# Kernel tuning notes

Hardware: AMD Instinct MI355X
Metric: run time of the kernel (lower is better)

Reference implementation:

```python
import jax, jax.numpy as jnp
import numpy as np
import math

B, T, C, H = 2, 2048, 1024, 16
D = C // H  # head dim = 64

def setup_inputs() -> dict:
    key = jax.random.key(0)
    ks = jax.random.split(key, 9)
    s = 0.02
    return {
        "x": jax.random.normal(ks[0], (B, T, C), dtype=jnp.float32),
        "Wq": jax.random.normal(ks[1], (C, C), dtype=jnp.float32) * s,
        "bq": jax.random.normal(ks[2], (C,), dtype=jnp.float32) * s,
        "Wk": jax.random.normal(ks[3], (C, C), dtype=jnp.float32) * s,
        "bk": jax.random.normal(ks[4], (C,), dtype=jnp.float32) * s,
        "Wv": jax.random.normal(ks[5], (C, C), dtype=jnp.float32) * s,
        "bv": jax.random.normal(ks[6], (C,), dtype=jnp.float32) * s,
        "Wo": jax.random.normal(ks[7], (C, C), dtype=jnp.float32) * s,
        "bo": jax.random.normal(ks[8], (C,), dtype=jnp.float32) * s,
    }

def reference(x, Wq, bq, Wk, bk, Wv, bv, Wo, bo):
    # x: [B, T, C]; torch Linear is y = x @ W.T + b
    Bv_, Tv_, Cv_ = x.shape
    q = (x @ Wq.T + bq).reshape(Bv_, Tv_, H, D)
    k = (x @ Wk.T + bk).reshape(Bv_, Tv_, H, D)
    v = (x @ Wv.T + bv).reshape(Bv_, Tv_, H, D)
    scale = 1.0 / math.sqrt(D)
    # [B, H, Tq, Tk] attention scores
    att = jnp.einsum("bqhd,bkhd->bhqk", q, k) * scale
    causal = jnp.tril(jnp.ones((Tv_, Tv_), dtype=bool))  # [T, T]
    att = jnp.where(causal[None, None, :, :], att, -jnp.inf)
    att = jax.nn.softmax(att, axis=-1)
    y = jnp.einsum("bhqk,bkhd->bqhd", att, v).reshape(Bv_, Tv_, Cv_)
    return y @ Wo.T + bo
```

## Files before the change

kernel.cpp:

```cpp
#include <hip/hip_runtime.h>
#include <hip/hip_bf16.h>
#include <cstdint>
#include <cstddef>

typedef __attribute__((ext_vector_type(8))) short short8;
typedef __attribute__((ext_vector_type(4))) float f32x4;
typedef unsigned int u32;
typedef __attribute__((ext_vector_type(4))) u32 u32x4;

#define MFMA(a,b,c) __builtin_amdgcn_mfma_f32_16x16x32_bf16(a,b,c,0,0,0)

__device__ __forceinline__ void gload_lds16(const void* gptr, void* lptr) {
  __builtin_amdgcn_global_load_lds((const __attribute__((address_space(1))) u32*)gptr,
                                   (__attribute__((address_space(3))) u32*)lptr, 16, 0, 0);
}

template<int N> __device__ __forceinline__ void vm_wait() {
  asm volatile("s_waitcnt vmcnt(%0)" :: "n"(N) : "memory");
}

__device__ __forceinline__ void barrier_sync() {
  asm volatile("" ::: "memory");
  __builtin_amdgcn_s_barrier();
  asm volatile("" ::: "memory");
  __builtin_amdgcn_sched_barrier(0);
}

__device__ __forceinline__ unsigned short f2bf(float f) {
  __hip_bfloat16 h = __float2bfloat16(f);
  return *reinterpret_cast<unsigned short*>(&h);
}

__device__ __forceinline__ short8 ldg8(const unsigned short* p) {
  return *reinterpret_cast<const short8*>(p);
}

__device__ __forceinline__ u32 cvt_pk_bf16(float lo, float hi) {
  u32 r;
  asm("v_cvt_pk_bf16_f32 %0, %1, %2" : "=v"(r) : "v"(lo), "v"(hi));
  return r;
}

__global__ __launch_bounds__(256) void cvt_all_kernel(
    const float* __restrict__ x,
    const float* __restrict__ w0, const float* __restrict__ w1,
    const float* __restrict__ w2, const float* __restrict__ w3,
    unsigned short* __restrict__ xb,
    unsigned short* __restrict__ o0, unsigned short* __restrict__ o1,
    unsigned short* __restrict__ o2, unsigned short* __restrict__ o3)
{
  int id = blockIdx.x * blockDim.x + threadIdx.x;
  const float* in;
  unsigned short* out;
  int idx;
  if (id < 1048576) {
    in = x; out = xb; idx = id;
  } else {
    int r = id - 1048576;
    int z = r >> 18;
    idx = r & 262143;
    in  = (z == 0) ? w0 : (z == 1) ? w1 : (z == 2) ? w2 : w3;
    out = (z == 0) ? o0 : (z == 1) ? o1 : (z == 2) ? o2 : o3;
  }
  float4 f = reinterpret_cast<const float4*>(in)[idx];
  ushort4 o;
  o.x = f2bf(f.x); o.y = f2bf(f.y); o.z = f2bf(f.z); o.w = f2bf(f.w);
  reinterpret_cast<ushort4*>(out)[idx] = o;
}

template<int BM, int BN, int WM, int WN, bool F32OUT>
__device__ __forceinline__ void gemm2_body(
    const unsigned short* __restrict__ A,
    const unsigned short* __restrict__ W,
    const float* __restrict__ bias,
    unsigned short* __restrict__ outb, float* __restrict__ outf,
    int ldo, float oscale, int m0)
{
  constexpr int K = 1024, BK = 32, NT = K / BK;
  constexpr int NTHR = WM * WN * 64;
  constexpr int FM = BM / (WM * 16);
  constexpr int FN = BN / (WN * 16);
  constexpr int NLA = BM * BK * 2 / (NTHR * 16);
  constexpr int NLB = BN * BK * 2 / (NTHR * 16);
  constexpr int NLD = NLA + NLB;

  __shared__ unsigned short As[2][BM * BK];
  __shared__ unsigned short Ws[2][BN * BK];

  const int tid = threadIdx.x;
  const int lane = tid & 63;
  const int wave = tid >> 6;
  const int wm = wave / WN, wn = wave % WN;
  const int wr = wm * FM * 16, wc = wn * FN * 16;
  const int lr = lane >> 4, lc = lane & 15;

  f32x4 acc[FM][FN] = {};

  const char* Ab = (const char*)(A + (size_t)m0 * K);
  const char* Wb = (const char*)W;

#define STAGE(buf, k0)                                                            \
  {                                                                               \
    _Pragma("unroll")                                                             \
    for (int i = 0; i < NLA; ++i) {                                               \
      int L = (i * NTHR + tid) * 16;                                              \
      int row = L >> 6;                                                           \
      int col = L & 63;                                                           \
      gload_lds16(Ab + (size_t)row * 2048 + (k0) * 2 + col, (char*)&As[buf][0] + L); \
    }                                                                             \
    _Pragma("unroll")                                                             \
    for (int i = 0; i < NLB; ++i) {                                               \
      int L = (i * NTHR + tid) * 16;                                              \
      int row = L >> 6;                                                           \
      int col = L & 63;                                                           \
      gload_lds16(Wb + (size_t)row * 2048 + (k0) * 2 + col, (char*)&Ws[buf][0] + L); \
    }                                                                             \
  }

#define COMPUTE(buf)                                                              \
  {                                                                               \
    short8 af[FM], bf[FN];                                                        \
    _Pragma("unroll")                                                             \
    for (int m = 0; m < FM; ++m) {                                                \
      int row = wr + m * 16 + lc;                                                 \
      af[m] = *reinterpret_cast<const short8*>(                                   \
          (const char*)&As[buf][0] + row * 64 + lr * 16);                         \
    }                                                                             \
    _Pragma("unroll")                                                             \
    for (int n = 0; n < FN; ++n) {                                                \
      int row = wc + n * 16 + lc;                                                 \
      bf[n] = *reinterpret_cast<const short8*>(                                   \
          (const char*)&Ws[buf][0] + row * 64 + lr * 16);                         \
    }                                                                             \
    __builtin_amdgcn_s_setprio(1);                                                \
    _Pragma("unroll")                                                             \
    for (int m = 0; m < FM; ++m)                                                  \
      _Pragma("unroll")                                                           \
      for (int n = 0; n < FN; ++n)                                                \
        acc[m][n] = MFMA(af[m], bf[n], acc[m][n]);                                \
    __builtin_amdgcn_s_setprio(0);                                                \
  }

  STAGE(0, 0)
  STAGE(1, BK)
  int cur = 0;
#pragma unroll 1
  for (int kt = 0; kt < NT - 2; ++kt) {
    vm_wait<NLD>();
    barrier_sync();
    COMPUTE(cur)
    barrier_sync();
    STAGE(cur, (kt + 2) * BK)
    cur ^= 1;
  }
  vm_wait<NLD>();
  barrier_sync();
  COMPUTE(cur)
  cur ^= 1;
  vm_wait<0>();
  barrier_sync();
  COMPUTE(cur)

#undef STAGE
#undef COMPUTE

#pragma unroll
  for (int m = 0; m < FM; ++m)
#pragma unroll
    for (int n = 0; n < FN; ++n)
#pragma unroll
      for (int r = 0; r < 4; ++r) {
        int row = m0 + wr + m * 16 + lr * 4 + r;
        int col = wc + n * 16 + lc;
        float v = (acc[m][n][r] + bias[col]) * oscale;
        if (F32OUT) outf[(size_t)row * ldo + col] = v;
        else        outb[(size_t)row * ldo + col] = f2bf(v);
      }
}

__global__ __launch_bounds__(256, 3) void gemm_qkv5(
    const unsigned short* __restrict__ xb,
    const unsigned short* __restrict__ Wqb, const unsigned short* __restrict__ Wkb,
    const unsigned short* __restrict__ Wvb,
    const float* __restrict__ bq, const float* __restrict__ bk, const float* __restrict__ bv,
    unsigned short* __restrict__ Q, unsigned short* __restrict__ Ko, unsigned short* __restrict__ V)
{
  const int i = blockIdx.x;
  const int sw = (i & 7) * 96 + (i >> 3);
  const int z  = sw >> 8;
  const int rr = sw & 255;
  const int m0 = (rr >> 3) * 128;
  const int nr = (rr & 7) * 128;
  const unsigned short* W = ((z == 0) ? Wqb : (z == 1) ? Wkb : Wvb) + (size_t)nr * 1024;
  const float* bias = ((z == 0) ? bq : (z == 1) ? bk : bv) + nr;
  unsigned short* out = ((z == 0) ? Q : (z == 1) ? Ko : V) + nr;
  const float oscale = (z == 0) ? 0.18033688011112042f : 1.0f;
  gemm2_body<128, 128, 2, 2, false>(xb, W, bias, out, nullptr, 1024, oscale, m0);
}

__global__ __launch_bounds__(256, 2) void gemm_out3(
    const unsigned short* __restrict__ Y, const unsigned short* __restrict__ Wob,
    const float* __restrict__ bo, float* __restrict__ out)
{
  const int i = blockIdx.x;
  const int sw = (i & 7) * 64 + (i >> 3);
  const int by = sw >> 3;
  const int bx = sw & 7;
  const int m0 = by * 64;
  const int n0 = bx * 128;
  gemm2_body<64, 128, 2, 2, true>(Y, Wob + (size_t)n0 * 1024, bo + n0, nullptr, out + n0,
                                  1024, 1.0f, m0);
}

__global__ __launch_bounds__(256) void transpose_v(const unsigned short* __restrict__ V,
                                                   unsigned short* __restrict__ VT)
{
  __shared__ unsigned short tile[64 * 68];
  const int tb = blockIdx.x;
  const int bh = blockIdx.y;
  const int b = bh >> 4, h = bh & 15;
  const int tid = threadIdx.x;
  const int t0 = tb * 64;
#pragma unroll
  for (int i = 0; i < 4; ++i) {
    int e = (i * 256 + tid) * 4;
    int t = e >> 6, d = e & 63;
    ushort4 v = *reinterpret_cast<const ushort4*>(&V[((size_t)(b * 2048 + t0 + t)) * 1024 + h * 64 + d]);
    tile[t * 68 + d + 0] = v.x;
    tile[t * 68 + d + 1] = v.y;
    tile[t * 68 + d + 2] = v.z;
    tile[t * 68 + d + 3] = v.w;
  }
  __syncthreads();
#pragma unroll
  for (int i = 0; i < 4; ++i) {
    int e = (i * 256 + tid) * 4;
    int d = e >> 6, tc = e & 63;
    ushort4 w;
    w.x = tile[(tc + 0) * 68 + d];
    w.y = tile[(tc + 1) * 68 + d];
    w.z = tile[(tc + 2) * 68 + d];
    w.w = tile[(tc + 3) * 68 + d];
    *reinterpret_cast<ushort4*>(&VT[((size_t)(bh * 64 + d)) * 2048 + t0 + tc]) = w;
  }
}

__global__ __launch_bounds__(256) void attn_kernel(
    const unsigned short* __restrict__ Q, const unsigned short* __restrict__ K,
    const unsigned short* __restrict__ VT, unsigned short* __restrict__ Y)
{
  __shared__ unsigned short Ks[2][64 * 64];
  __shared__ unsigned short Vs[2][64 * 64];
  __shared__ u32 Pl[4][584];

  const int i   = blockIdx.x;
  const int xcd = i & 7;
  const int j   = i >> 3;
  const int bh  = xcd + 8 * (j & 3);
  const int qb  = 31 - (j >> 2);
  const int b = bh >> 4, h = bh & 15;
  const int tid = threadIdx.x;
  const int wave = tid >> 6;
  const int lane = tid & 63;
  const int lr = lane >> 4;
  const int lc = lane & 15;
  const float M = 4.0f;

  const unsigned short* Kbh = K + (size_t)b * 2048 * 1024 + h * 64;
  const unsigned short* Vbh = VT + (size_t)bh * 64 * 2048;
  u32* pw = Pl[wave];

  u32 ov = 0x3F803F80u;
  u32x4 ones4 = {ov, ov, ov, ov};
  short8 ones = *reinterpret_cast<short8*>(&ones4);

  const int q0 = qb * 64 + wave * 16;
  const unsigned short* qp = &Q[((size_t)(b * 2048 + q0 + lc)) * 1024 + h * 64 + lr * 8];
  short8 qa0 = ldg8(qp);
  short8 qa1 = ldg8(qp + 32);

  f32x4 o[4] = {};
  f32x4 lacc = {};

  const int nt = qb + 1;
  int cur = 0;

#pragma unroll
  for (int ii = 0; ii < 2; ++ii) {
    int L = (ii * 256 + tid) * 16;
    int row = L >> 7;
    int src = (L & 127) ^ ((row & 7) << 4);
    gload_lds16((const char*)(Kbh + (size_t)row * 1024) + src, (char*)&Ks[0][0] + L);
    gload_lds16((const char*)(Vbh + (size_t)row * 2048) + src, (char*)&Vs[0][0] + L);
  }
  __syncthreads();

  for (int t = 0; t < nt; ++t) {
    if (t + 1 < nt) {
      const int tk1 = (t + 1) * 64;
#pragma unroll
      for (int ii = 0; ii < 2; ++ii) {
        int L = (ii * 256 + tid) * 16;
        int row = L >> 7;
        int src = (L & 127) ^ ((row & 7) << 4);
        gload_lds16((const char*)(Kbh + (size_t)(tk1 + row) * 1024) + src, (char*)&Ks[cur ^ 1][0] + L);
        gload_lds16((const char*)(Vbh + (size_t)row * 2048 + tk1) + src, (char*)&Vs[cur ^ 1][0] + L);
      }
    }

    const int tk0 = t * 64;
    const unsigned short* Kt = Ks[cur];
    const unsigned short* Vt = Vs[cur];

    f32x4 s[4] = {};
#pragma unroll
    for (int kt = 0; kt < 4; ++kt) {
      int row = kt * 16 + lc;
      int sw = (row & 7) << 4;
      short8 kb0 = *reinterpret_cast<const short8*>((const char*)Kt + row * 128 + ((lr * 16) ^ sw));
      short8 kb1 = *reinterpret_cast<const short8*>((const char*)Kt + row * 128 + ((64 + lr * 16) ^ sw));
      __builtin_amdgcn_s_setprio(1);
      s[kt] = MFMA(kb0, qa0, s[kt]);
      s[kt] = MFMA(kb1, qa1, s[kt]);
      __builtin_amdgcn_s_setprio(0);
    }

    const bool diag = (t == qb);
    float p[4][4];
#pragma unroll
    for (int kt = 0; kt < 4; ++kt)
#pragma unroll
      for (int r = 0; r < 4; ++r)
        p[kt][r] = __builtin_amdgcn_exp2f(s[kt][r] - M);
    if (diag) {
#pragma unroll
      for (int kt = 0; kt < 4; ++kt)
#pragma unroll
        for (int r = 0; r < 4; ++r)
          if (tk0 + kt * 16 + lr * 4 + r > q0 + lc) p[kt][r] = 0.f;
    }

#pragma unroll
    for (int kt = 0; kt < 4; ++kt) {
      uint2 w;
      w.x = cvt_pk_bf16(p[kt][0], p[kt][1]);
      w.y = cvt_pk_bf16(p[kt][2], p[kt][3]);
      *reinterpret_cast<uint2*>(&pw[lc * 36 + kt * 8 + lr * 2]) = w;
    }
    short8 pa0 = *reinterpret_cast<const short8*>(&pw[lc * 36 + lr * 4]);
    short8 pa1 = *reinterpret_cast<const short8*>(&pw[lc * 36 + 16 + lr * 4]);

    __builtin_amdgcn_s_setprio(1);
    lacc = MFMA(pa0, ones, lacc);
    lacc = MFMA(pa1, ones, lacc);
    __builtin_amdgcn_s_setprio(0);

#pragma unroll
    for (int ntt = 0; ntt < 4; ++ntt) {
      int row = ntt * 16 + lc;
      int sw = (row & 7) << 4;
      short8 v0 = *reinterpret_cast<const short8*>((const char*)Vt + row * 128 + ((lr * 16) ^ sw));
      short8 v1 = *reinterpret_cast<const short8*>((const char*)Vt + row * 128 + ((64 + lr * 16) ^ sw));
      __builtin_amdgcn_s_setprio(1);
      o[ntt] = MFMA(pa0, v0, o[ntt]);
      o[ntt] = MFMA(pa1, v1, o[ntt]);
      __builtin_amdgcn_s_setprio(0);
    }

    __syncthreads();
    cur ^= 1;
  }

  float rl[4];
#pragma unroll
  for (int r = 0; r < 4; ++r) rl[r] = __builtin_amdgcn_rcpf(lacc[r]);
#pragma unroll
  for (int ntt = 0; ntt < 4; ++ntt)
#pragma unroll
    for (int r = 0; r < 4; ++r) {
      float val = o[ntt][r] * rl[r];
      int row = b * 2048 + q0 + lr * 4 + r;
      Y[(size_t)row * 1024 + h * 64 + ntt * 16 + lc] = f2bf(val);
    }
}

extern "C" void kernel_launch(void* const* d_in, const int* in_sizes, int n_in,
                              void* d_out, int out_size, void* d_ws, size_t ws_size,
                              hipStream_t stream)
{
  const float* x  = (const float*)d_in[0];
  const float* Wq = (const float*)d_in[1];
  const float* bq = (const float*)d_in[2];
  const float* Wk = (const float*)d_in[3];
  const float* bk = (const float*)d_in[4];
  const float* Wv = (const float*)d_in[5];
  const float* bv = (const float*)d_in[6];
  const float* Wo = (const float*)d_in[7];
  const float* bo = (const float*)d_in[8];
  float* out = (float*)d_out;

  char* ws = (char*)d_ws;
  unsigned short* xb  = (unsigned short*)(ws);
  unsigned short* Wqb = (unsigned short*)(ws + 8388608);
  unsigned short* Wkb = (unsigned short*)(ws + 8388608 + 2097152);
  unsigned short* Wvb = (unsigned short*)(ws + 8388608 + 2 * 2097152);
  unsigned short* Wob = (unsigned short*)(ws + 8388608 + 3 * 2097152);
  unsigned short* Qb  = (unsigned short*)(ws + 16777216);
  unsigned short* Kb  = (unsigned short*)(ws + 16777216 + 8388608);
  unsigned short* Vb  = (unsigned short*)(ws + 16777216 + 2 * 8388608);
  unsigned short* VTb = (unsigned short*)(ws + 16777216 + 3 * 8388608);
  unsigned short* Yb  = (unsigned short*)(ws + 16777216 + 4 * 8388608);

  cvt_all_kernel<<<8192, 256, 0, stream>>>(x, Wq, Wk, Wv, Wo, xb, Wqb, Wkb, Wvb, Wob);

  gemm_qkv5<<<768, 256, 0, stream>>>(xb, Wqb, Wkb, Wvb, bq, bk, bv, Qb, Kb, Vb);
  transpose_v<<<dim3(32, 32), 256, 0, stream>>>(Vb, VTb);
  attn_kernel<<<1024, 256, 0, stream>>>(Qb, Kb, VTb, Yb);
  gemm_out3<<<512, 256, 0, stream>>>(Yb, Wob, bo, out);
}
```

Before: 105.9 us.

## Rewrite attention with 32x32 MFMA, 128-query blocks and register P transpose

The attention kernel moves from 16x16x32 to 32x32x16 bf16 MFMA, with each wave owning 32 queries and each block 128 queries, so the grid drops from 1024 to 512 blocks. P is transposed into the B-operand layout in registers with permlane32_swap instead of going through LDS. The row sum is accumulated in scalar adds rather than a ones-MFMA. The q-block order is interleaved to balance the causal work, and launch bounds request three blocks per CU. The aim is to halve K/V LDS traffic per query and remove the LDS round trip for P. The cost is more registers per thread and fewer blocks to fill the GPU.

Measured after the change: 111.7 us. 5.5% more time.

```diff
diff --git a/kernel.cpp b/kernel.cpp
--- a/kernel.cpp
+++ b/kernel.cpp
@@ -5,10 +5,13 @@
 
 typedef __attribute__((ext_vector_type(8))) short short8;
 typedef __attribute__((ext_vector_type(4))) float f32x4;
+typedef __attribute__((ext_vector_type(16))) float f32x16;
 typedef unsigned int u32;
+typedef __attribute__((ext_vector_type(2))) u32 u32x2;
 typedef __attribute__((ext_vector_type(4))) u32 u32x4;
 
 #define MFMA(a,b,c) __builtin_amdgcn_mfma_f32_16x16x32_bf16(a,b,c,0,0,0)
+#define MFMA32(a,b,c) __builtin_amdgcn_mfma_f32_32x32x16_bf16(a,b,c,0,0,0)
 
 __device__ __forceinline__ void gload_lds16(const void* gptr, void* lptr) {
   __builtin_amdgcn_global_load_lds((const __attribute__((address_space(1))) u32*)gptr,
@@ -39,6 +42,11 @@
   u32 r;
   asm("v_cvt_pk_bf16_f32 %0, %1, %2" : "=v"(r) : "v"(lo), "v"(hi));
   return r;
+}
+
+__device__ __forceinline__ void plane32_swap(u32& a, u32& b) {
+  u32x2 r = __builtin_amdgcn_permlane32_swap(a, b, false, false);
+  a = r.x; b = r.y;
 }
 
 __global__ __launch_bounds__(256) void cvt_all_kernel(
@@ -245,143 +253,159 @@
   }
 }
 
-__global__ __launch_bounds__(256) void attn_kernel(
+__global__ __launch_bounds__(256, 3) void attn_kernel(
     const unsigned short* __restrict__ Q, const unsigned short* __restrict__ K,
     const unsigned short* __restrict__ VT, unsigned short* __restrict__ Y)
 {
   __shared__ unsigned short Ks[2][64 * 64];
   __shared__ unsigned short Vs[2][64 * 64];
-  __shared__ u32 Pl[4][584];
 
   const int i   = blockIdx.x;
   const int xcd = i & 7;
-  const int j   = i >> 3;
-  const int bh  = xcd + 8 * (j & 3);
-  const int qb  = 31 - (j >> 2);
+  const int bh  = xcd + 8 * ((i >> 3) & 3);
+  const int jj  = i >> 5;
+  const int qb  = (jj < 8) ? (15 - jj) : (jj - 8);
   const int b = bh >> 4, h = bh & 15;
   const int tid = threadIdx.x;
   const int wave = tid >> 6;
   const int lane = tid & 63;
-  const int lr = lane >> 4;
-  const int lc = lane & 15;
+  const int ql = lane & 31;
+  const int hi = lane >> 5;
   const float M = 4.0f;
 
   const unsigned short* Kbh = K + (size_t)b * 2048 * 1024 + h * 64;
   const unsigned short* Vbh = VT + (size_t)bh * 64 * 2048;
-  u32* pw = Pl[wave];
-
-  u32 ov = 0x3F803F80u;
-  u32x4 ones4 = {ov, ov, ov, ov};
-  short8 ones = *reinterpret_cast<short8*>(&ones4);
-
-  const int q0 = qb * 64 + wave * 16;
-  const unsigned short* qp = &Q[((size_t)(b * 2048 + q0 + lc)) * 1024 + h * 64 + lr * 8];
-  short8 qa0 = ldg8(qp);
-  short8 qa1 = ldg8(qp + 32);
-
-  f32x4 o[4] = {};
-  f32x4 lacc = {};
-
-  const int nt = qb + 1;
+
+  const int q0w = qb * 128 + wave * 32;
+  const int qg  = q0w + ql;
+
+  short8 qf[4];
+  {
+    const unsigned short* qp = &Q[((size_t)(b * 2048 + qg)) * 1024 + h * 64 + hi * 8];
+#pragma unroll
+    for (int kk = 0; kk < 4; ++kk) qf[kk] = ldg8(qp + kk * 16);
+  }
+
+  f32x16 o0 = {}, o1 = {};
+  float lacc = 0.f;
+
+  const int nt = 2 * qb + 2;
+
+#define STAGE_KV(buf, t)                                                          \
+  {                                                                               \
+    const int tk = (t) * 64;                                                      \
+    _Pragma("unroll")                                                             \
+    for (int ii = 0; ii < 2; ++ii) {                                              \
+      int L = (ii * 256 + tid) * 16;                                              \
+      int row = L >> 7;                                                           \
+      int src = (L & 127) ^ ((row & 7) << 4);                                     \
+      gload_lds16((const char*)(Kbh + (size_t)(tk + row) * 1024) + src,           \
+                  (char*)&Ks[buf][0] + L);                                        \
+      gload_lds16((const char*)(Vbh + (size_t)row * 2048 + tk) + src,             \
+                  (char*)&Vs[buf][0] + L);                                        \
+    }                                                                             \
+  }
+
+  STAGE_KV(0, 0)
+  __syncthreads();
   int cur = 0;
-
-#pragma unroll
-  for (int ii = 0; ii < 2; ++ii) {
-    int L = (ii * 256 + tid) * 16;
-    int row = L >> 7;
-    int src = (L & 127) ^ ((row & 7) << 4);
-    gload_lds16((const char*)(Kbh + (size_t)row * 1024) + src, (char*)&Ks[0][0] + L);
-    gload_lds16((const char*)(Vbh + (size_t)row * 2048) + src, (char*)&Vs[0][0] + L);
-  }
-  __syncthreads();
-
+#pragma unroll 1
   for (int t = 0; t < nt; ++t) {
-    if (t + 1 < nt) {
-      const int tk1 = (t + 1) * 64;
-#pragma unroll
-      for (int ii = 0; ii < 2; ++ii) {
-        int L = (ii * 256 + tid) * 16;
-        int row = L >> 7;
-        int src = (L & 127) ^ ((row & 7) << 4);
-        gload_lds16((const char*)(Kbh + (size_t)(tk1 + row) * 1024) + src, (char*)&Ks[cur ^ 1][0] + L);
-        gload_lds16((const char*)(Vbh + (size_t)row * 2048 + tk1) + src, (char*)&Vs[cur ^ 1][0] + L);
+    if (t + 1 < nt) STAGE_KV(cur ^ 1, t + 1)
+
+    const int tk0 = t * 64;
+    if (tk0 <= q0w + 31) {
+      const char* Kt = (const char*)&Ks[cur][0];
+      const char* Vt = (const char*)&Vs[cur][0];
+
+      f32x16 sa0 = {}, sa1 = {};
+#pragma unroll
+      for (int kk = 0; kk < 4; ++kk) {
+        int krow0 = ql;
+        int krow1 = 32 + ql;
+        int off = kk * 32 + hi * 16;
+        short8 ka0 = *reinterpret_cast<const short8*>(Kt + krow0 * 128 + (off ^ ((krow0 & 7) << 4)));
+        short8 ka1 = *reinterpret_cast<const short8*>(Kt + krow1 * 128 + (off ^ ((krow1 & 7) << 4)));
+        __builtin_amdgcn_s_setprio(1);
+        sa0 = MFMA32(ka0, qf[kk], sa0);
+        sa1 = MFMA32(ka1, qf[kk], sa1);
+        __builtin_amdgcn_s_setprio(0);
+      }
+
+      const bool needMask = (tk0 + 63 > q0w);
+      short8 pb[4];
+#pragma unroll
+      for (int kpos = 0; kpos < 2; ++kpos) {
+        const f32x16& sa = kpos ? sa1 : sa0;
+        const int kbase = tk0 + kpos * 32;
+        float p[16];
+#pragma unroll
+        for (int r = 0; r < 16; ++r)
+          p[r] = __builtin_amdgcn_exp2f(sa[r] - M);
+        if (needMask) {
+#pragma unroll
+          for (int r = 0; r < 16; ++r) {
+            int kg = kbase + (r & 3) + 8 * (r >> 2) + 4 * hi;
+            if (kg > qg) p[r] = 0.f;
+          }
+        }
+#pragma unroll
+        for (int r = 0; r < 16; ++r) lacc += p[r];
+        {
+          u32 a0 = cvt_pk_bf16(p[0], p[1]), b0 = cvt_pk_bf16(p[4], p[5]);
+          u32 a1 = cvt_pk_bf16(p[2], p[3]), b1 = cvt_pk_bf16(p[6], p[7]);
+          plane32_swap(a0, b0);
+          plane32_swap(a1, b1);
+          u32x4 w = {a0, a1, b0, b1};
+          pb[2 * kpos + 0] = *reinterpret_cast<short8*>(&w);
+        }
+        {
+          u32 a0 = cvt_pk_bf16(p[8], p[9]),  b0 = cvt_pk_bf16(p[12], p[13]);
+          u32 a1 = cvt_pk_bf16(p[10], p[11]), b1 = cvt_pk_bf16(p[14], p[15]);
+          plane32_swap(a0, b0);
+          plane32_swap(a1, b1);
+          u32x4 w = {a0, a1, b0, b1};
+          pb[2 * kpos + 1] = *reinterpret_cast<short8*>(&w);
+        }
+      }
+
+#pragma unroll
+      for (int kk = 0; kk < 4; ++kk) {
+        int drow0 = ql;
+        int drow1 = 32 + ql;
+        int off = kk * 32 + hi * 16;
+        short8 va0 = *reinterpret_cast<const short8*>(Vt + drow0 * 128 + (off ^ ((drow0 & 7) << 4)));
+        short8 va1 = *reinterpret_cast<const short8*>(Vt + drow1 * 128 + (off ^ ((drow1 & 7) << 4)));
+        __builtin_amdgcn_s_setprio(1);
+        o0 = MFMA32(va0, pb[kk], o0);
+        o1 = MFMA32(va1, pb[kk], o1);
+        __builtin_amdgcn_s_setprio(0);
       }
     }
 
-    const int tk0 = t * 64;
-    const unsigned short* Kt = Ks[cur];
-    const unsigned short* Vt = Vs[cur];
-
-    f32x4 s[4] = {};
-#pragma unroll
-    for (int kt = 0; kt < 4; ++kt) {
-      int row = kt * 16 + lc;
-      int sw = (row & 7) << 4;
-      short8 kb0 = *reinterpret_cast<const short8*>((const char*)Kt + row * 128 + ((lr * 16) ^ sw));
-      short8 kb1 = *reinterpret_cast<const short8*>((const char*)Kt + row * 128 + ((64 + lr * 16) ^ sw));
-      __builtin_amdgcn_s_setprio(1);
-      s[kt] = MFMA(kb0, qa0, s[kt]);
-      s[kt] = MFMA(kb1, qa1, s[kt]);
-      __builtin_amdgcn_s_setprio(0);
-    }
-
-    const bool diag = (t == qb);
-    float p[4][4];
-#pragma unroll
-    for (int kt = 0; kt < 4; ++kt)
-#pragma unroll
-      for (int r = 0; r < 4; ++r)
-        p[kt][r] = __builtin_amdgcn_exp2f(s[kt][r] - M);
-    if (diag) {
-#pragma unroll
-      for (int kt = 0; kt < 4; ++kt)
-#pragma unroll
-        for (int r = 0; r < 4; ++r)
-          if (tk0 + kt * 16 + lr * 4 + r > q0 + lc) p[kt][r] = 0.f;
-    }
-
-#pragma unroll
-    for (int kt = 0; kt < 4; ++kt) {
-      uint2 w;
-      w.x = cvt_pk_bf16(p[kt][0], p[kt][1]);
-      w.y = cvt_pk_bf16(p[kt][2], p[kt][3]);
-      *reinterpret_cast<uint2*>(&pw[lc * 36 + kt * 8 + lr * 2]) = w;
-    }
-    short8 pa0 = *reinterpret_cast<const short8*>(&pw[lc * 36 + lr * 4]);
-    short8 pa1 = *reinterpret_cast<const short8*>(&pw[lc * 36 + 16 + lr * 4]);
-
-    __builtin_amdgcn_s_setprio(1);
-    lacc = MFMA(pa0, ones, lacc);
-    lacc = MFMA(pa1, ones, lacc);
-    __builtin_amdgcn_s_setprio(0);
-
-#pragma unroll
-    for (int ntt = 0; ntt < 4; ++ntt) {
-      int row = ntt * 16 + lc;
-      int sw = (row & 7) << 4;
-      short8 v0 = *reinterpret_cast<const short8*>((const char*)Vt + row * 128 + ((lr * 16) ^ sw));
-      short8 v1 = *reinterpret_cast<const short8*>((const char*)Vt + row * 128 + ((64 + lr * 16) ^ sw));
-      __builtin_amdgcn_s_setprio(1);
-      o[ntt] = MFMA(pa0, v0, o[ntt]);
-      o[ntt] = MFMA(pa1, v1, o[ntt]);
-      __builtin_amdgcn_s_setprio(0);
-    }
-
     __syncthreads();
     cur ^= 1;
   }
 
-  float rl[4];
-#pragma unroll
-  for (int r = 0; r < 4; ++r) rl[r] = __builtin_amdgcn_rcpf(lacc[r]);
-#pragma unroll
-  for (int ntt = 0; ntt < 4; ++ntt)
-#pragma unroll
-    for (int r = 0; r < 4; ++r) {
-      float val = o[ntt][r] * rl[r];
-      int row = b * 2048 + q0 + lr * 4 + r;
-      Y[(size_t)row * 1024 + h * 64 + ntt * 16 + lc] = f2bf(val);
+#undef STAGE_KV
+
+  lacc += __shfl_xor(lacc, 32);
+  float rl = __builtin_amdgcn_rcpf(lacc);
+  unsigned short* yrow = &Y[((size_t)(b * 2048 + qg)) * 1024 + h * 64];
+#pragma unroll
+  for (int dpos = 0; dpos < 2; ++dpos) {
+    const f32x16& o = dpos ? o1 : o0;
+#pragma unroll
+    for (int rq = 0; rq < 16; rq += 4) {
+      ushort4 w;
+      w.x = f2bf(o[rq + 0] * rl);
+      w.y = f2bf(o[rq + 1] * rl);
+      w.z = f2bf(o[rq + 2] * rl);
+      w.w = f2bf(o[rq + 3] * rl);
+      int d0 = dpos * 32 + 8 * (rq >> 2) + 4 * hi;
+      *reinterpret_cast<ushort4*>(yrow + d0) = w;
     }
+  }
 }
 
 extern "C" void kernel_launch(void* const* d_in, const int* in_sizes, int n_in,
@@ -415,6 +439,6 @@
 
   gemm_qkv5<<<768, 256, 0, stream>>>(xb, Wqb, Wkb, Wvb, bq, bk, bv, Qb, Kb, Vb);
   transpose_v<<<dim3(32, 32), 256, 0, stream>>>(Vb, VTb);
-  attn_kernel<<<1024, 256, 0, stream>>>(Qb, Kb, VTb, Yb);
+  attn_kernel<<<512, 256, 0, stream>>>(Qb, Kb, VTb, Yb);
   gemm_out3<<<512, 256, 0, stream>>>(Yb, Wob, bo, out);
 }
```
